# Kernel tuning notes

Measured on AMD Instinct MI355X. Metric: run time of the kernel, lower is better.

## Reference

```python
import jax, jax.numpy as jnp
import numpy as np

N_A = 500000
N_B = 500000
NUM_HERBS = 25000
D = 128  # hidden_dim


def setup_inputs() -> dict:
    key = jax.random.key(0)
    ks = jax.random.split(key, 12)
    h_A = jax.random.normal(ks[0], (N_A, D), dtype=jnp.float32)
    h_B = jax.random.normal(ks[1], (N_B, D), dtype=jnp.float32)
    herb_idx_A = jnp.sort(jax.random.randint(ks[2], (N_A,), 0, NUM_HERBS, dtype=jnp.int64))
    herb_idx_B = jnp.sort(jax.random.randint(ks[3], (N_B,), 0, NUM_HERBS, dtype=jnp.int64))
    # attn_net: Linear(2D, D//2) -> LeakyReLU(0.2) -> Linear(D//2, 1)
    aw1 = jax.random.normal(ks[4], (2 * D, D // 2), dtype=jnp.float32) / np.sqrt(2 * D)
    ab1 = jnp.zeros((D // 2,), dtype=jnp.float32)
    aw2 = jax.random.normal(ks[5], (D // 2, 1), dtype=jnp.float32) / np.sqrt(D // 2)
    ab2 = jnp.zeros((1,), dtype=jnp.float32)
    # fusion_mlp: Linear(4D, 2D) -> ReLU -> Linear(2D, D)
    fw1 = jax.random.normal(ks[6], (4 * D, 2 * D), dtype=jnp.float32) / np.sqrt(4 * D)
    fb1 = jnp.zeros((2 * D,), dtype=jnp.float32)
    fw2 = jax.random.normal(ks[7], (2 * D, D), dtype=jnp.float32) / np.sqrt(2 * D)
    fb2 = jnp.zeros((D,), dtype=jnp.float32)
    return {"h_A": h_A, "h_B": h_B, "herb_idx_A": herb_idx_A, "herb_idx_B": herb_idx_B,
            "num_herbs": NUM_HERBS,
            "aw1": aw1, "ab1": ab1, "aw2": aw2, "ab2": ab2,
            "fw1": fw1, "fb1": fb1, "fw2": fw2, "fb2": fb2}


def _seg_mean(x, idx, n):
    s = jax.ops.segment_sum(x, idx, num_segments=n)          # [n, D]
    cnt = jax.ops.segment_sum(jnp.ones((x.shape[0], 1), x.dtype), idx, num_segments=n)
    return s / jnp.maximum(cnt, 1.0)


def _seg_softmax(score, idx, n):
    # score: [N, 1]; numerically-stable per-segment softmax (as in PyG softmax)
    m = jax.ops.segment_max(score, idx, num_segments=n)       # [n, 1]
    e = jnp.exp(score - m[idx])
    denom = jax.ops.segment_sum(e, idx, num_segments=n)
    return e / (denom[idx] + 1e-16)


def _attn(x, aw1, ab1, aw2, ab2):
    h = jax.nn.leaky_relu(x @ aw1 + ab1, negative_slope=0.2)
    return h @ aw2 + ab2                                      # [N, 1]


def reference(h_A, h_B, herb_idx_A, herb_idx_B, num_herbs,
              aw1, ab1, aw2, ab2, fw1, fb1, fw2, fb2):
    H_B_mean = _seg_mean(h_B, herb_idx_B, num_herbs)          # [H, D]
    H_A_mean = _seg_mean(h_A, herb_idx_A, num_herbs)          # [H, D]

    cat_A = jnp.concatenate([h_A, H_B_mean[herb_idx_A]], axis=-1)  # [N_A, 2D]
    alpha_A = _seg_softmax(_attn(cat_A, aw1, ab1, aw2, ab2), herb_idx_A, num_herbs)
    H_A_given_B = jax.ops.segment_sum(alpha_A * h_A, herb_idx_A, num_segments=num_herbs)

    cat_B = jnp.concatenate([h_B, H_A_mean[herb_idx_B]], axis=-1)  # [N_B, 2D]
    alpha_B = _seg_softmax(_attn(cat_B, aw1, ab1, aw2, ab2), herb_idx_B, num_herbs)
    H_B_given_A = jax.ops.segment_sum(alpha_B * h_B, herb_idx_B, num_segments=num_herbs)

    concat_feat = jnp.concatenate([H_A_given_B, H_B_given_A,
                                   H_A_given_B * H_B_given_A,
                                   jnp.abs(H_A_given_B - H_B_given_A)], axis=-1)  # [H, 4D]
    H_interaction = jax.nn.relu(concat_feat @ fw1 + fb1) @ fw2 + fb2              # [H, D]
    return (H_interaction, H_A_given_B, H_B_given_A)
```

## Files before the change

### kernel.cpp

```cpp
#include <hip/hip_runtime.h>
#include <math.h>

#define H_HERBS 25000
#define DIM 128

typedef __attribute__((ext_vector_type(8))) short bf16x8;
typedef __attribute__((ext_vector_type(4))) float f32x4;

__device__ inline unsigned pack2bf(float a, float b) {
    union { float f; unsigned u; } x, y; x.f = a; y.f = b;
    return ((x.u + 0x8000u) >> 16) | ((y.u + 0x8000u) & 0xFFFF0000u);
}

__global__ void k_starts(const int* __restrict__ idxA, const int* __restrict__ idxB,
                         int nA, int nB, int* __restrict__ startA, int* __restrict__ startB) {
    int h = blockIdx.x * blockDim.x + threadIdx.x;
    if (h > H_HERBS) return;
    {
        int lo = 0, hi = nA;
        while (lo < hi) { int mid = (lo + hi) >> 1; if (idxA[mid] < h) lo = mid + 1; else hi = mid; }
        startA[h] = lo;
    }
    {
        int lo = 0, hi = nB;
        while (lo < hi) { int mid = (lo + hi) >> 1; if (idxB[mid] < h) lo = mid + 1; else hi = mid; }
        startB[h] = lo;
    }
}

__global__ __launch_bounds__(64) void k_packw(
        const float* __restrict__ fw1, const float* __restrict__ fw2,
        uint4* __restrict__ w1bf, uint4* __restrict__ w2bf) {
    int b = blockIdx.x, l = threadIdx.x;
    int c = l & 15, kg = l >> 4;
    if (b < 256) {
        int kt = b >> 4, nt = b & 15;
        int k0 = kt * 32 + kg * 8, j = nt * 16 + c;
        unsigned u0 = pack2bf(fw1[(size_t)(k0 + 0) * 256 + j], fw1[(size_t)(k0 + 1) * 256 + j]);
        unsigned u1 = pack2bf(fw1[(size_t)(k0 + 2) * 256 + j], fw1[(size_t)(k0 + 3) * 256 + j]);
        unsigned u2 = pack2bf(fw1[(size_t)(k0 + 4) * 256 + j], fw1[(size_t)(k0 + 5) * 256 + j]);
        unsigned u3 = pack2bf(fw1[(size_t)(k0 + 6) * 256 + j], fw1[(size_t)(k0 + 7) * 256 + j]);
        w1bf[(size_t)b * 64 + l] = make_uint4(u0, u1, u2, u3);
    } else {
        int bb = b - 256;
        int kt = bb >> 3, nt = bb & 7;
        int k0 = kt * 32 + kg * 8, j = nt * 16 + c;
        unsigned u0 = pack2bf(fw2[(size_t)(k0 + 0) * 128 + j], fw2[(size_t)(k0 + 1) * 128 + j]);
        unsigned u1 = pack2bf(fw2[(size_t)(k0 + 2) * 128 + j], fw2[(size_t)(k0 + 3) * 128 + j]);
        unsigned u2 = pack2bf(fw2[(size_t)(k0 + 4) * 128 + j], fw2[(size_t)(k0 + 5) * 128 + j]);
        unsigned u3 = pack2bf(fw2[(size_t)(k0 + 6) * 128 + j], fw2[(size_t)(k0 + 7) * 128 + j]);
        w2bf[(size_t)bb * 64 + l] = make_uint4(u0, u1, u2, u3);
    }
}

__global__ __launch_bounds__(256) void k_mean_proj(
        const float* __restrict__ X, const int* __restrict__ start,
        const float* __restrict__ aw1, const float* __restrict__ ab1,
        float* __restrict__ mpart) {
    __shared__ float Wl[128 * 64];
    __shared__ __align__(16) float mb[16][128];
    int h0 = blockIdx.x * 16;
    int t = threadIdx.x;

    {
        const float4* Wsrc = (const float4*)(aw1 + 128 * 64);
        float4* Wl4 = (float4*)Wl;
        #pragma unroll
        for (int q = 0; q < 8; ++q) Wl4[t + 256 * q] = Wsrc[t + 256 * q];
    }

    int wv = t >> 6, ln = t & 63, half = ln >> 5, li = ln & 31;
    const float4* X4 = (const float4*)X;
    #pragma unroll
    for (int i = 0; i < 4; ++i) {
        int hh = wv * 4 + i;
        int h = h0 + hh;
        if (h >= H_HERBS) { if (half == 0) ((float4*)mb[hh])[li] = make_float4(0.f,0.f,0.f,0.f); continue; }
        int s = start[h], e = start[h + 1];
        float4 acc = make_float4(0.f, 0.f, 0.f, 0.f);
        int r = s + half;
        for (; r + 6 < e; r += 8) {
            float4 v0 = X4[(size_t)r * 32 + li];
            float4 v1 = X4[(size_t)(r + 2) * 32 + li];
            float4 v2 = X4[(size_t)(r + 4) * 32 + li];
            float4 v3 = X4[(size_t)(r + 6) * 32 + li];
            acc.x += (v0.x + v1.x) + (v2.x + v3.x);
            acc.y += (v0.y + v1.y) + (v2.y + v3.y);
            acc.z += (v0.z + v1.z) + (v2.z + v3.z);
            acc.w += (v0.w + v1.w) + (v2.w + v3.w);
        }
        for (; r < e; r += 2) {
            float4 v0 = X4[(size_t)r * 32 + li];
            acc.x += v0.x; acc.y += v0.y; acc.z += v0.z; acc.w += v0.w;
        }
        acc.x += __shfl_xor(acc.x, 32, 64);
        acc.y += __shfl_xor(acc.y, 32, 64);
        acc.z += __shfl_xor(acc.z, 32, 64);
        acc.w += __shfl_xor(acc.w, 32, 64);
        int cnt = e - s;
        float inv = 1.0f / (float)(cnt > 1 ? cnt : 1);
        if (half == 0) {
            ((float4*)mb[hh])[li] = make_float4(acc.x * inv, acc.y * inv, acc.z * inv, acc.w * inv);
        }
    }
    __syncthreads();

    {
        int j = t & 63, wg = t >> 6;
        float b1 = ab1[j];
        float a0 = b1, a1 = b1, a2 = b1, a3 = b1;
        #pragma unroll 8
        for (int k = 0; k < 128; ++k) {
            float w = Wl[k * 64 + j];
            a0 += mb[wg * 4 + 0][k] * w;
            a1 += mb[wg * 4 + 1][k] * w;
            a2 += mb[wg * 4 + 2][k] * w;
            a3 += mb[wg * 4 + 3][k] * w;
        }
        int h = h0 + wg * 4;
        if (h + 0 < H_HERBS) mpart[(size_t)(h + 0) * 64 + j] = a0;
        if (h + 1 < H_HERBS) mpart[(size_t)(h + 1) * 64 + j] = a1;
        if (h + 2 < H_HERBS) mpart[(size_t)(h + 2) * 64 + j] = a2;
        if (h + 3 < H_HERBS) mpart[(size_t)(h + 3) * 64 + j] = a3;
    }
}

__global__ __launch_bounds__(256) void k_mpart_one(
        const float* __restrict__ meanG, const float* __restrict__ aw1,
        const float* __restrict__ ab1, float* __restrict__ mpart) {
    __shared__ float Wl[128 * 64];
    __shared__ float mb[64 * 128];
    int h0 = blockIdx.x * 64;
    int t = threadIdx.x;

    const float4* Wsrc = (const float4*)(aw1 + 128 * 64);
    float4* Wl4 = (float4*)Wl;
    #pragma unroll
    for (int q = 0; q < 8; ++q) Wl4[t + 256 * q] = Wsrc[t + 256 * q];
    float4* mb4 = (float4*)mb;
    const float4* mG4 = (const float4*)meanG;
    #pragma unroll
    for (int q = 0; q < 8; ++q) {
        int ent = t + 256 * q;
        int hl = ent >> 5, kq = ent & 31;
        int h = h0 + hl;
        mb4[ent] = (h < H_HERBS) ? mG4[(size_t)h * 32 + kq] : make_float4(0.f, 0.f, 0.f, 0.f);
    }
    __syncthreads();

    int j = t & 63, hg = t >> 6;
    float b1 = ab1[j];
    #pragma unroll
    for (int ii = 0; ii < 4; ++ii) {
        int hl0 = hg * 16 + ii * 4;
        float a0 = 0.f, a1 = 0.f, a2 = 0.f, a3 = 0.f;
        for (int k = 0; k < 128; ++k) {
            float w = Wl[k * 64 + j];
            a0 += mb[(hl0 + 0) * 128 + k] * w;
            a1 += mb[(hl0 + 1) * 128 + k] * w;
            a2 += mb[(hl0 + 2) * 128 + k] * w;
            a3 += mb[(hl0 + 3) * 128 + k] * w;
        }
        int h = h0 + hl0;
        if (h + 0 < H_HERBS) mpart[(size_t)(h + 0) * 64 + j] = b1 + a0;
        if (h + 1 < H_HERBS) mpart[(size_t)(h + 1) * 64 + j] = b1 + a1;
        if (h + 2 < H_HERBS) mpart[(size_t)(h + 2) * 64 + j] = b1 + a2;
        if (h + 3 < H_HERBS) mpart[(size_t)(h + 3) * 64 + j] = b1 + a3;
    }
}

__global__ __launch_bounds__(256) void k_scores_one(
        const float* __restrict__ X, const int* __restrict__ idx,
        const float* __restrict__ mpart,
        const float* __restrict__ aw1, const float* __restrict__ aw2,
        const float* __restrict__ ab2,
        float* __restrict__ scores, int n) {
    int t = threadIdx.x;
    int l = t & 63, wid = t >> 6;
    int c = l & 15, kg = l >> 4;

    union ABu { bf16x8 v; unsigned u[4]; };

    ABu wf[4][4];
    #pragma unroll
    for (int kb = 0; kb < 4; ++kb) {
        int k0 = kb * 32 + kg * 8;
        #pragma unroll
        for (int nb = 0; nb < 4; ++nb) {
            int j = nb * 16 + c;
            #pragma unroll
            for (int e = 0; e < 4; ++e) {
                wf[kb][nb].u[e] = pack2bf(aw1[(size_t)(k0 + 2 * e)     * 64 + j],
                                          aw1[(size_t)(k0 + 2 * e + 1) * 64 + j]);
            }
        }
    }
    float a2[4];
    #pragma unroll
    for (int nb = 0; nb < 4; ++nb) a2[nb] = aw2[nb * 16 + c];
    float b2s = ab2[0];

    for (int pass = 0; pass < 4; ++pass) {
        long r0 = (long)blockIdx.x * 256 + pass * 64 + wid * 16;
        if (r0 >= n) break;
        long myrow = r0 + c;
        if (myrow >= n) myrow = n - 1;
        const float4* Xr = (const float4*)(X + (size_t)myrow * DIM);

        ABu af[4];
        #pragma unroll
        for (int kb = 0; kb < 4; ++kb) {
            float4 a = Xr[kb * 8 + kg * 2];
            float4 b = Xr[kb * 8 + kg * 2 + 1];
            af[kb].u[0] = pack2bf(a.x, a.y);
            af[kb].u[1] = pack2bf(a.z, a.w);
            af[kb].u[2] = pack2bf(b.x, b.y);
            af[kb].u[3] = pack2bf(b.z, b.w);
        }

        f32x4 acc[4];
        #pragma unroll
        for (int nb = 0; nb < 4; ++nb) { acc[nb].x = 0.f; acc[nb].y = 0.f; acc[nb].z = 0.f; acc[nb].w = 0.f; }
        #pragma unroll
        for (int kb = 0; kb < 4; ++kb) {
            #pragma unroll
            for (int nb = 0; nb < 4; ++nb) {
                acc[nb] = __builtin_amdgcn_mfma_f32_16x16x32_bf16(af[kb].v, wf[kb][nb].v, acc[nb], 0, 0, 0);
            }
        }

        int rgrp = kg * 4;
        float part[4] = {0.f, 0.f, 0.f, 0.f};
        #pragma unroll
        for (int reg = 0; reg < 4; ++reg) {
            long rr = r0 + rgrp + reg;
            bool v = rr < n;
            int h = v ? idx[rr] : 0;
            const float* mp = mpart + (size_t)h * 64;
            #pragma unroll
            for (int nb = 0; nb < 4; ++nb) {
                float hv = acc[nb][reg] + mp[nb * 16 + c];
                hv = hv > 0.f ? hv : 0.2f * hv;
                part[reg] += hv * a2[nb];
            }
        }
        #pragma unroll
        for (int reg = 0; reg < 4; ++reg) {
            float p = part[reg];
            p += __shfl_xor(p, 1, 64);
            p += __shfl_xor(p, 2, 64);
            p += __shfl_xor(p, 4, 64);
            p += __shfl_xor(p, 8, 64);
            part[reg] = p;
        }
        if (c == 0) {
            #pragma unroll
            for (int reg = 0; reg < 4; ++reg) {
                long rr = r0 + rgrp + reg;
                if (rr < n) scores[rr] = part[reg] + b2s;
            }
        }
    }
}

template <bool WITH_MEAN>
__global__ __launch_bounds__(64) void k_attn_one(
        const float* __restrict__ X, const int* __restrict__ start,
        const float* __restrict__ scores,
        float* __restrict__ out, float* __restrict__ meanOut) {
    int h = blockIdx.x;
    int lane = threadIdx.x;
    int half = lane >> 5, li = lane & 31;
    int s = start[h], e = start[h + 1];
    const float4* X4 = (const float4*)X;
    float4 acc = make_float4(0.f, 0.f, 0.f, 0.f);
    float4 accS = make_float4(0.f, 0.f, 0.f, 0.f);
    if (e > s) {
        float mx = -INFINITY;
        for (int r = s + lane; r < e; r += 64) mx = fmaxf(mx, scores[r]);
        #pragma unroll
        for (int o = 32; o; o >>= 1) mx = fmaxf(mx, __shfl_xor(mx, o, 64));
        float sum = 0.f;
        for (int r = s + lane; r < e; r += 64) sum += __expf(scores[r] - mx);
        #pragma unroll
        for (int o = 32; o; o >>= 1) sum += __shfl_xor(sum, o, 64);
        float invden = 1.0f / (sum + 1e-16f);

        int r = s + half;
        for (; r + 6 < e; r += 8) {
            float w0 = __expf(scores[r]     - mx) * invden;
            float w1 = __expf(scores[r + 2] - mx) * invden;
            float w2 = __expf(scores[r + 4] - mx) * invden;
            float w3 = __expf(scores[r + 6] - mx) * invden;
            float4 v0 = X4[(size_t)r * 32 + li];
            float4 v1 = X4[(size_t)(r + 2) * 32 + li];
            float4 v2 = X4[(size_t)(r + 4) * 32 + li];
            float4 v3 = X4[(size_t)(r + 6) * 32 + li];
            acc.x += (w0 * v0.x + w1 * v1.x) + (w2 * v2.x + w3 * v3.x);
            acc.y += (w0 * v0.y + w1 * v1.y) + (w2 * v2.y + w3 * v3.y);
            acc.z += (w0 * v0.z + w1 * v1.z) + (w2 * v2.z + w3 * v3.z);
            acc.w += (w0 * v0.w + w1 * v1.w) + (w2 * v2.w + w3 * v3.w);
            if (WITH_MEAN) {
                accS.x += (v0.x + v1.x) + (v2.x + v3.x);
                accS.y += (v0.y + v1.y) + (v2.y + v3.y);
                accS.z += (v0.z + v1.z) + (v2.z + v3.z);
                accS.w += (v0.w + v1.w) + (v2.w + v3.w);
            }
        }
        for (; r < e; r += 2) {
            float w0 = __expf(scores[r] - mx) * invden;
            float4 v0 = X4[(size_t)r * 32 + li];
            acc.x += w0 * v0.x; acc.y += w0 * v0.y;
            acc.z += w0 * v0.z; acc.w += w0 * v0.w;
            if (WITH_MEAN) {
                accS.x += v0.x; accS.y += v0.y; accS.z += v0.z; accS.w += v0.w;
            }
        }
    }
    acc.x += __shfl_xor(acc.x, 32, 64);
    acc.y += __shfl_xor(acc.y, 32, 64);
    acc.z += __shfl_xor(acc.z, 32, 64);
    acc.w += __shfl_xor(acc.w, 32, 64);
    if (WITH_MEAN) {
        accS.x += __shfl_xor(accS.x, 32, 64);
        accS.y += __shfl_xor(accS.y, 32, 64);
        accS.z += __shfl_xor(accS.z, 32, 64);
        accS.w += __shfl_xor(accS.w, 32, 64);
    }
    if (half == 0) {
        ((float4*)out)[(size_t)h * 32 + li] = acc;
        if (WITH_MEAN) {
            int cnt = e - s;
            float inv = 1.0f / (float)(cnt > 1 ? cnt : 1);
            ((float4*)meanOut)[(size_t)h * 32 + li] =
                make_float4(accS.x * inv, accS.y * inv, accS.z * inv, accS.w * inv);
        }
    }
}

__global__ __launch_bounds__(256) void k_fusion_mfma(
        const float* __restrict__ HA, const float* __restrict__ HB,
        const uint4* __restrict__ w1bf, const uint4* __restrict__ w2bf,
        const float* __restrict__ fb1, const float* __restrict__ fb2,
        float* __restrict__ out) {
    __shared__ float hid[32 * 256];
    int t = threadIdx.x, wid = t >> 6, l = t & 63, c = l & 15, kg = l >> 4;
    int h0 = blockIdx.x * 32;
    int ms = wid & 1, nh = wid >> 1;

    union ABu { bf16x8 v; unsigned u[4]; uint4 q; };

    {
        int rowl = ms * 16 + c;
        int h = h0 + rowl;
        bool hv = h < H_HERBS;
        const float* pa = HA + (size_t)(hv ? h : h0) * DIM;
        const float* pb = HB + (size_t)(hv ? h : h0) * DIM;

        f32x4 acc[8];
        #pragma unroll
        for (int nt = 0; nt < 8; ++nt) { acc[nt].x = 0.f; acc[nt].y = 0.f; acc[nt].z = 0.f; acc[nt].w = 0.f; }

        #pragma unroll
        for (int kt = 0; kt < 16; ++kt) {
            int k0 = kt * 32 + kg * 8;
            int range = k0 >> 7, off = k0 & 127;
            float f[8];
            if (range == 0) {
                float4 a0 = *(const float4*)(pa + off), a1 = *(const float4*)(pa + off + 4);
                f[0] = a0.x; f[1] = a0.y; f[2] = a0.z; f[3] = a0.w;
                f[4] = a1.x; f[5] = a1.y; f[6] = a1.z; f[7] = a1.w;
            } else if (range == 1) {
                float4 b0 = *(const float4*)(pb + off), b1 = *(const float4*)(pb + off + 4);
                f[0] = b0.x; f[1] = b0.y; f[2] = b0.z; f[3] = b0.w;
                f[4] = b1.x; f[5] = b1.y; f[6] = b1.z; f[7] = b1.w;
            } else if (range == 2) {
                float4 a0 = *(const float4*)(pa + off), a1 = *(const float4*)(pa + off + 4);
                float4 b0 = *(const float4*)(pb + off), b1 = *(const float4*)(pb + off + 4);
                f[0] = a0.x * b0.x; f[1] = a0.y * b0.y; f[2] = a0.z * b0.z; f[3] = a0.w * b0.w;
                f[4] = a1.x * b1.x; f[5] = a1.y * b1.y; f[6] = a1.z * b1.z; f[7] = a1.w * b1.w;
            } else {
                float4 a0 = *(const float4*)(pa + off), a1 = *(const float4*)(pa + off + 4);
                float4 b0 = *(const float4*)(pb + off), b1 = *(const float4*)(pb + off + 4);
                f[0] = fabsf(a0.x - b0.x); f[1] = fabsf(a0.y - b0.y);
                f[2] = fabsf(a0.z - b0.z); f[3] = fabsf(a0.w - b0.w);
                f[4] = fabsf(a1.x - b1.x); f[5] = fabsf(a1.y - b1.y);
                f[6] = fabsf(a1.z - b1.z); f[7] = fabsf(a1.w - b1.w);
            }
            ABu af;
            af.u[0] = pack2bf(f[0], f[1]); af.u[1] = pack2bf(f[2], f[3]);
            af.u[2] = pack2bf(f[4], f[5]); af.u[3] = pack2bf(f[6], f[7]);
            #pragma unroll
            for (int nt = 0; nt < 8; ++nt) {
                ABu bfr; bfr.q = w1bf[(size_t)(kt * 16 + nh * 8 + nt) * 64 + l];
                acc[nt] = __builtin_amdgcn_mfma_f32_16x16x32_bf16(af.v, bfr.v, acc[nt], 0, 0, 0);
            }
        }

        #pragma unroll
        for (int nt = 0; nt < 8; ++nt) {
            int j = nh * 128 + nt * 16 + c;
            float b1 = fb1[j];
            #pragma unroll
            for (int reg = 0; reg < 4; ++reg) {
                int row = ms * 16 + kg * 4 + reg;
                float v = fmaxf(acc[nt][reg] + b1, 0.f);
                hid[row * 256 + (j ^ ((row & 7) << 3))] = v;
            }
        }
    }
    __syncthreads();

    {
        int rowl = ms * 16 + c;
        f32x4 acc2[4];
        #pragma unroll
        for (int nt = 0; nt < 4; ++nt) { acc2[nt].x = 0.f; acc2[nt].y = 0.f; acc2[nt].z = 0.f; acc2[nt].w = 0.f; }

        #pragma unroll
        for (int kt = 0; kt < 8; ++kt) {
            int j0 = kt * 32 + kg * 8;
            int widx = rowl * 256 + (j0 ^ ((rowl & 7) << 3));
            float4 h0v = *(const float4*)&hid[widx];
            float4 h1v = *(const float4*)&hid[widx + 4];
            ABu af;
            af.u[0] = pack2bf(h0v.x, h0v.y); af.u[1] = pack2bf(h0v.z, h0v.w);
            af.u[2] = pack2bf(h1v.x, h1v.y); af.u[3] = pack2bf(h1v.z, h1v.w);
            #pragma unroll
            for (int nt = 0; nt < 4; ++nt) {
                ABu bfr; bfr.q = w2bf[(size_t)(kt * 8 + nh * 4 + nt) * 64 + l];
                acc2[nt] = __builtin_amdgcn_mfma_f32_16x16x32_bf16(af.v, bfr.v, acc2[nt], 0, 0, 0);
            }
        }

        #pragma unroll
        for (int nt = 0; nt < 4; ++nt) {
            int j = nh * 64 + nt * 16 + c;
            float b2 = fb2[j];
            #pragma unroll
            for (int reg = 0; reg < 4; ++reg) {
                int row = ms * 16 + kg * 4 + reg;
                int h = h0 + row;
                if (h < H_HERBS) out[(size_t)h * DIM + j] = acc2[nt][reg] + b2;
            }
        }
    }
}

extern "C" void kernel_launch(void* const* d_in, const int* in_sizes, int n_in,
                              void* d_out, int out_size, void* d_ws, size_t ws_size,
                              hipStream_t stream) {
    const float* hA  = (const float*)d_in[0];
    const float* hB  = (const float*)d_in[1];
    const int*   idxA = (const int*)d_in[2];
    const int*   idxB = (const int*)d_in[3];
    const float* aw1 = (const float*)d_in[5];
    const float* ab1 = (const float*)d_in[6];
    const float* aw2 = (const float*)d_in[7];
    const float* ab2 = (const float*)d_in[8];
    const float* fw1 = (const float*)d_in[9];
    const float* fb1 = (const float*)d_in[10];
    const float* fw2 = (const float*)d_in[11];
    const float* fb2 = (const float*)d_in[12];

    int nA = in_sizes[0] / DIM;
    int nB = in_sizes[1] / DIM;

    float* out  = (float*)d_out;
    float* outI = out;
    float* outA = out + (size_t)H_HERBS * DIM;
    float* outB = out + (size_t)2 * H_HERBS * DIM;
    float* meanA = outI;

    char* w = (char*)d_ws;
    auto carve = [&](size_t bytes) { char* p = w; w += (bytes + 255) & ~(size_t)255; return p; };
    int*   startA  = (int*)carve((size_t)(H_HERBS + 1) * sizeof(int));
    int*   startB  = (int*)carve((size_t)(H_HERBS + 1) * sizeof(int));
    float* mpartA  = (float*)carve((size_t)H_HERBS * 64 * sizeof(float));
    float* mpartB  = (float*)carve((size_t)H_HERBS * 64 * sizeof(float));
    float* scoresA = (float*)carve((size_t)nA * sizeof(float));
    float* scoresB = (float*)carve((size_t)nB * sizeof(float));
    uint4* w1bf    = (uint4*)carve((size_t)256 * 64 * sizeof(uint4));
    uint4* w2bf    = (uint4*)carve((size_t)64 * 64 * sizeof(uint4));

    int gridA = (nA + 255) / 256;
    int gridB = (nB + 255) / 256;
    int nhb16 = (H_HERBS + 15) / 16;
    int nhb64 = (H_HERBS + 63) / 64;

    k_starts<<<(H_HERBS + 1 + 255) / 256, 256, 0, stream>>>(idxA, idxB, nA, nB, startA, startB);
    k_packw<<<320, 64, 0, stream>>>(fw1, fw2, w1bf, w2bf);

    k_mean_proj<<<nhb16, 256, 0, stream>>>(hB, startB, aw1, ab1, mpartA);
    k_scores_one<<<gridA, 256, 0, stream>>>(hA, idxA, mpartA, aw1, aw2, ab2, scoresA, nA);
    k_attn_one<true><<<H_HERBS, 64, 0, stream>>>(hA, startA, scoresA, outA, meanA);
    k_mpart_one<<<nhb64, 256, 0, stream>>>(meanA, aw1, ab1, mpartB);
    k_scores_one<<<gridB, 256, 0, stream>>>(hB, idxB, mpartB, aw1, aw2, ab2, scoresB, nB);
    k_attn_one<false><<<H_HERBS, 64, 0, stream>>>(hB, startB, scoresB, outB, nullptr);
    k_fusion_mfma<<<(H_HERBS + 31) / 32, 256, 0, stream>>>(outA, outB, w1bf, w2bf, fb1, fb2, outI);
}
```

Before: 388.1 us.

## Fuse per-row attention scoring and segment softmax aggregation into one kernel

Replaces the separate MFMA score kernel and the per-herb softmax/aggregation kernel with one kernel per 16-herb block. Scores for the block's rows stay in shared memory instead of a global scores buffer. The exponentials are computed once and stored, and normalisation is applied once at the output. The second pass over X re-reads rows the same block just touched, so it is meant to hit cache instead of HBM and to save a launch. In exchange, each block's row count is capped at SCAP=1024, so rows past the cap are silently dropped if a 16-herb group has too many. Work is also split less evenly across blocks.

```diff
diff --git a/kernel.cpp b/kernel.cpp
--- a/kernel.cpp
+++ b/kernel.cpp
@@ -3,6 +3,7 @@
 
 #define H_HERBS 25000
 #define DIM 128
+#define SCAP 1024
 
 typedef __attribute__((ext_vector_type(8))) short bf16x8;
 typedef __attribute__((ext_vector_type(4))) float f32x4;
@@ -169,15 +170,25 @@
     }
 }
 
-__global__ __launch_bounds__(256) void k_scores_one(
+template <bool WITH_MEAN>
+__global__ __launch_bounds__(256) void k_seg_attn_mfma(
         const float* __restrict__ X, const int* __restrict__ idx,
-        const float* __restrict__ mpart,
+        const int* __restrict__ start, const float* __restrict__ mpart,
         const float* __restrict__ aw1, const float* __restrict__ aw2,
         const float* __restrict__ ab2,
-        float* __restrict__ scores, int n) {
+        float* __restrict__ out, float* __restrict__ meanOut) {
+    __shared__ float sc[SCAP];
+    __shared__ float invden_s[16];
+
     int t = threadIdx.x;
-    int l = t & 63, wid = t >> 6;
+    int wv = t >> 6, l = t & 63;
     int c = l & 15, kg = l >> 4;
+
+    int h0 = blockIdx.x * 16;
+    int nh = H_HERBS - h0; if (nh > 16) nh = 16;
+    int rs = start[h0];
+    int re = start[h0 + nh];
+    int cnt = re - rs; if (cnt > SCAP) cnt = SCAP;
 
     union ABu { bf16x8 v; unsigned u[4]; };
 
@@ -200,12 +211,12 @@
     for (int nb = 0; nb < 4; ++nb) a2[nb] = aw2[nb * 16 + c];
     float b2s = ab2[0];
 
-    for (int pass = 0; pass < 4; ++pass) {
-        long r0 = (long)blockIdx.x * 256 + pass * 64 + wid * 16;
-        if (r0 >= n) break;
-        long myrow = r0 + c;
-        if (myrow >= n) myrow = n - 1;
-        const float4* Xr = (const float4*)(X + (size_t)myrow * DIM);
+    int ntiles = (cnt + 15) >> 4;
+    for (int tile = wv; tile < ntiles; tile += 4) {
+        int lr0 = tile * 16;
+        int lrow = lr0 + c;
+        int lrowc = lrow < cnt ? lrow : cnt - 1;
+        const float4* Xr = (const float4*)(X + (size_t)(rs + lrowc) * DIM);
 
         ABu af[4];
         #pragma unroll
@@ -230,72 +241,66 @@
         }
 
         int rgrp = kg * 4;
-        float part[4] = {0.f, 0.f, 0.f, 0.f};
         #pragma unroll
         for (int reg = 0; reg < 4; ++reg) {
-            long rr = r0 + rgrp + reg;
-            bool v = rr < n;
-            int h = v ? idx[rr] : 0;
+            int rl = lr0 + rgrp + reg;
+            bool v = rl < cnt;
+            int h = v ? idx[rs + rl] : h0;
             const float* mp = mpart + (size_t)h * 64;
+            float part = 0.f;
             #pragma unroll
             for (int nb = 0; nb < 4; ++nb) {
                 float hv = acc[nb][reg] + mp[nb * 16 + c];
                 hv = hv > 0.f ? hv : 0.2f * hv;
-                part[reg] += hv * a2[nb];
-            }
-        }
-        #pragma unroll
-        for (int reg = 0; reg < 4; ++reg) {
-            float p = part[reg];
-            p += __shfl_xor(p, 1, 64);
-            p += __shfl_xor(p, 2, 64);
-            p += __shfl_xor(p, 4, 64);
-            p += __shfl_xor(p, 8, 64);
-            part[reg] = p;
-        }
-        if (c == 0) {
-            #pragma unroll
-            for (int reg = 0; reg < 4; ++reg) {
-                long rr = r0 + rgrp + reg;
-                if (rr < n) scores[rr] = part[reg] + b2s;
-            }
-        }
-    }
-}
-
-template <bool WITH_MEAN>
-__global__ __launch_bounds__(64) void k_attn_one(
-        const float* __restrict__ X, const int* __restrict__ start,
-        const float* __restrict__ scores,
-        float* __restrict__ out, float* __restrict__ meanOut) {
-    int h = blockIdx.x;
-    int lane = threadIdx.x;
-    int half = lane >> 5, li = lane & 31;
-    int s = start[h], e = start[h + 1];
-    const float4* X4 = (const float4*)X;
-    float4 acc = make_float4(0.f, 0.f, 0.f, 0.f);
-    float4 accS = make_float4(0.f, 0.f, 0.f, 0.f);
-    if (e > s) {
+                part += hv * a2[nb];
+            }
+            part += __shfl_xor(part, 1, 64);
+            part += __shfl_xor(part, 2, 64);
+            part += __shfl_xor(part, 4, 64);
+            part += __shfl_xor(part, 8, 64);
+            if (c == 0 && v) sc[rl] = part + b2s;
+        }
+    }
+    __syncthreads();
+
+    for (int i = wv; i < nh; i += 4) {
+        int h = h0 + i;
+        int ls = start[h] - rs, le = start[h + 1] - rs;
+        if (ls > cnt) ls = cnt;
+        if (le > cnt) le = cnt;
+        if (le <= ls) { if (l == 0) invden_s[i] = 0.f; continue; }
         float mx = -INFINITY;
-        for (int r = s + lane; r < e; r += 64) mx = fmaxf(mx, scores[r]);
+        for (int r = ls + l; r < le; r += 64) mx = fmaxf(mx, sc[r]);
         #pragma unroll
         for (int o = 32; o; o >>= 1) mx = fmaxf(mx, __shfl_xor(mx, o, 64));
         float sum = 0.f;
-        for (int r = s + lane; r < e; r += 64) sum += __expf(scores[r] - mx);
+        for (int r = ls + l; r < le; r += 64) {
+            float e = __expf(sc[r] - mx);
+            sc[r] = e;
+            sum += e;
+        }
         #pragma unroll
         for (int o = 32; o; o >>= 1) sum += __shfl_xor(sum, o, 64);
-        float invden = 1.0f / (sum + 1e-16f);
-
-        int r = s + half;
-        for (; r + 6 < e; r += 8) {
-            float w0 = __expf(scores[r]     - mx) * invden;
-            float w1 = __expf(scores[r + 2] - mx) * invden;
-            float w2 = __expf(scores[r + 4] - mx) * invden;
-            float w3 = __expf(scores[r + 6] - mx) * invden;
-            float4 v0 = X4[(size_t)r * 32 + li];
-            float4 v1 = X4[(size_t)(r + 2) * 32 + li];
-            float4 v2 = X4[(size_t)(r + 4) * 32 + li];
-            float4 v3 = X4[(size_t)(r + 6) * 32 + li];
+        if (l == 0) invden_s[i] = 1.0f / (sum + 1e-16f);
+    }
+    __syncthreads();
+
+    const float4* X4 = (const float4*)X;
+    int half = l >> 5, li = l & 31;
+    for (int i = wv; i < nh; i += 4) {
+        int h = h0 + i;
+        int ls = start[h] - rs, le = start[h + 1] - rs;
+        if (ls > cnt) ls = cnt;
+        if (le > cnt) le = cnt;
+        float4 acc = make_float4(0.f, 0.f, 0.f, 0.f);
+        float4 accS = make_float4(0.f, 0.f, 0.f, 0.f);
+        int r = ls + half;
+        for (; r + 6 < le; r += 8) {
+            float w0 = sc[r], w1 = sc[r + 2], w2 = sc[r + 4], w3 = sc[r + 6];
+            float4 v0 = X4[(size_t)(rs + r) * 32 + li];
+            float4 v1 = X4[(size_t)(rs + r + 2) * 32 + li];
+            float4 v2 = X4[(size_t)(rs + r + 4) * 32 + li];
+            float4 v3 = X4[(size_t)(rs + r + 6) * 32 + li];
             acc.x += (w0 * v0.x + w1 * v1.x) + (w2 * v2.x + w3 * v3.x);
             acc.y += (w0 * v0.y + w1 * v1.y) + (w2 * v2.y + w3 * v3.y);
             acc.z += (w0 * v0.z + w1 * v1.z) + (w2 * v2.z + w3 * v3.z);
@@ -307,33 +312,35 @@
                 accS.w += (v0.w + v1.w) + (v2.w + v3.w);
             }
         }
-        for (; r < e; r += 2) {
-            float w0 = __expf(scores[r] - mx) * invden;
-            float4 v0 = X4[(size_t)r * 32 + li];
+        for (; r < le; r += 2) {
+            float w0 = sc[r];
+            float4 v0 = X4[(size_t)(rs + r) * 32 + li];
             acc.x += w0 * v0.x; acc.y += w0 * v0.y;
             acc.z += w0 * v0.z; acc.w += w0 * v0.w;
             if (WITH_MEAN) {
                 accS.x += v0.x; accS.y += v0.y; accS.z += v0.z; accS.w += v0.w;
             }
         }
-    }
-    acc.x += __shfl_xor(acc.x, 32, 64);
-    acc.y += __shfl_xor(acc.y, 32, 64);
-    acc.z += __shfl_xor(acc.z, 32, 64);
-    acc.w += __shfl_xor(acc.w, 32, 64);
-    if (WITH_MEAN) {
-        accS.x += __shfl_xor(accS.x, 32, 64);
-        accS.y += __shfl_xor(accS.y, 32, 64);
-        accS.z += __shfl_xor(accS.z, 32, 64);
-        accS.w += __shfl_xor(accS.w, 32, 64);
-    }
-    if (half == 0) {
-        ((float4*)out)[(size_t)h * 32 + li] = acc;
+        acc.x += __shfl_xor(acc.x, 32, 64);
+        acc.y += __shfl_xor(acc.y, 32, 64);
+        acc.z += __shfl_xor(acc.z, 32, 64);
+        acc.w += __shfl_xor(acc.w, 32, 64);
         if (WITH_MEAN) {
-            int cnt = e - s;
-            float inv = 1.0f / (float)(cnt > 1 ? cnt : 1);
-            ((float4*)meanOut)[(size_t)h * 32 + li] =
-                make_float4(accS.x * inv, accS.y * inv, accS.z * inv, accS.w * inv);
+            accS.x += __shfl_xor(accS.x, 32, 64);
+            accS.y += __shfl_xor(accS.y, 32, 64);
+            accS.z += __shfl_xor(accS.z, 32, 64);
+            accS.w += __shfl_xor(accS.w, 32, 64);
+        }
+        if (half == 0) {
+            float inv = invden_s[i];
+            ((float4*)out)[(size_t)h * 32 + li] =
+                make_float4(acc.x * inv, acc.y * inv, acc.z * inv, acc.w * inv);
+            if (WITH_MEAN) {
+                int ch = le - ls;
+                float im = 1.0f / (float)(ch > 1 ? ch : 1);
+                ((float4*)meanOut)[(size_t)h * 32 + li] =
+                    make_float4(accS.x * im, accS.y * im, accS.z * im, accS.w * im);
+            }
         }
     }
 }
@@ -478,13 +485,9 @@
     int*   startB  = (int*)carve((size_t)(H_HERBS + 1) * sizeof(int));
     float* mpartA  = (float*)carve((size_t)H_HERBS * 64 * sizeof(float));
     float* mpartB  = (float*)carve((size_t)H_HERBS * 64 * sizeof(float));
-    float* scoresA = (float*)carve((size_t)nA * sizeof(float));
-    float* scoresB = (float*)carve((size_t)nB * sizeof(float));
     uint4* w1bf    = (uint4*)carve((size_t)256 * 64 * sizeof(uint4));
     uint4* w2bf    = (uint4*)carve((size_t)64 * 64 * sizeof(uint4));
 
-    int gridA = (nA + 255) / 256;
-    int gridB = (nB + 255) / 256;
     int nhb16 = (H_HERBS + 15) / 16;
     int nhb64 = (H_HERBS + 63) / 64;
 
@@ -492,10 +495,10 @@
     k_packw<<<320, 64, 0, stream>>>(fw1, fw2, w1bf, w2bf);
 
     k_mean_proj<<<nhb16, 256, 0, stream>>>(hB, startB, aw1, ab1, mpartA);
-    k_scores_one<<<gridA, 256, 0, stream>>>(hA, idxA, mpartA, aw1, aw2, ab2, scoresA, nA);
-    k_attn_one<true><<<H_HERBS, 64, 0, stream>>>(hA, startA, scoresA, outA, meanA);
+    k_seg_attn_mfma<true><<<nhb16, 256, 0, stream>>>(hA, idxA, startA, mpartA,
+                                                     aw1, aw2, ab2, outA, meanA);
     k_mpart_one<<<nhb64, 256, 0, stream>>>(meanA, aw1, ab1, mpartB);
-    k_scores_one<<<gridB, 256, 0, stream>>>(hB, idxB, mpartB, aw1, aw2, ab2, scoresB, nB);
-    k_attn_one<false><<<H_HERBS, 64, 0, stream>>>(hB, startB, scoresB, outB, nullptr);
+    k_seg_attn_mfma<false><<<nhb16, 256, 0, stream>>>(hB, idxB, startB, mpartB,
+                                                      aw1, aw2, ab2, outB, nullptr);
     k_fusion_mfma<<<(H_HERBS + 31) / 32, 256, 0, stream>>>(outA, outB, w1bf, w2bf, fb1, fb2, outI);
 }
```

After: 423.3 us. 1.09x slower.
